# Performance work log

Measured on AMD Instinct MI355X. Metric: run time of the kernel, lower is better.

The kernel has to match this reference:

```python
import jax, jax.numpy as jnp
import numpy as np

NUM_HEADS = 6
V = 25          # num_points (joints)
F = 64          # num_frames
T = F * V       # 1600 tokens
DIM = 216
HD = DIM // NUM_HEADS
SCALE = HD ** -0.5
MAX_HOP = 16    # hop-distance table size (distances clipped to MAX_HOP-1)
LN_EPS = 1e-5


def _ntu_hop_dist():
    # NTU RGB+D 25-joint skeleton edges (1-indexed)
    edges = [(1, 2), (2, 21), (3, 21), (4, 3), (5, 21), (6, 5), (7, 6), (8, 7),
             (9, 21), (10, 9), (11, 10), (12, 11), (13, 1), (14, 13), (15, 14),
             (16, 15), (17, 1), (18, 17), (19, 18), (20, 19), (22, 23), (23, 8),
             (24, 25), (25, 12)]
    D = np.full((V, V), 99, dtype=np.int64)
    np.fill_diagonal(D, 0)
    for a, b in edges:
        D[a - 1, b - 1] = 1
        D[b - 1, a - 1] = 1
    for k in range(V):  # Floyd-Warshall on tiny 25-node graph
        D = np.minimum(D, D[:, k:k + 1] + D[k:k + 1, :])
    return np.clip(D, 0, MAX_HOP - 1).astype(np.int32)


def setup_inputs() -> dict:
    key = jax.random.key(0)
    ks = jax.random.split(key, 16)
    s = 0.02  # trunc_normal_(std=0.02) init scale
    rn = lambda k, shape: jax.random.normal(k, shape, jnp.float32) * s
    return {
        "x": jax.random.normal(ks[0], (8, T, DIM), jnp.float32),
        "qkv_w": rn(ks[1], (3 * DIM, DIM)),
        "proj_w": rn(ks[2], (DIM, DIM)),
        "proj_b": jnp.zeros((DIM,), jnp.float32),
        "norm_w": jnp.ones((DIM,), jnp.float32),
        "norm_b": jnp.zeros((DIM,), jnp.float32),
        "norm1_w": jnp.ones((DIM,), jnp.float32),
        "norm1_b": jnp.zeros((DIM,), jnp.float32),
        "fc1_w": rn(ks[3], (4 * DIM, DIM)),
        "fc1_b": jnp.zeros((4 * DIM,), jnp.float32),
        "fc2_w": rn(ks[4], (DIM, 4 * DIM)),
        "fc2_b": jnp.zeros((DIM,), jnp.float32),
        "t_w1": rn(ks[5], (DIM, 1)),
        "t_b1": jnp.zeros((DIM,), jnp.float32),
        "t_w2": rn(ks[6], (NUM_HEADS, DIM)),
        "t_b2": jnp.zeros((NUM_HEADS,), jnp.float32),
        "h_w1": rn(ks[7], (DIM, 1)),
        "h_b1": jnp.zeros((DIM,), jnp.float32),
        "h_w2": rn(ks[8], (NUM_HEADS, DIM)),
        "h_b2": jnp.zeros((NUM_HEADS,), jnp.float32),
        "hop_dist": jnp.asarray(_ntu_hop_dist()),
    }


def _ln(x, w, b):
    mu = x.mean(-1, keepdims=True)
    var = jnp.mean((x - mu) ** 2, axis=-1, keepdims=True)
    return (x - mu) * jax.lax.rsqrt(var + LN_EPS) * w + b


def reference(x, qkv_w, proj_w, proj_b, norm_w, norm_b, norm1_w, norm1_b,
              fc1_w, fc1_b, fc2_w, fc2_b, t_w1, t_b1, t_w2, t_b2,
              h_w1, h_b1, h_w2, h_b2, hop_dist):
    N = x.shape[0]
    h = _ln(x, norm_w, norm_b)
    qkv = (h @ qkv_w.T).reshape(N, T, 3, NUM_HEADS, HD).transpose(2, 0, 3, 1, 4)
    q, k, v = qkv[0], qkv[1], qkv[2]                       # (N,H,T,HD)
    attn = jnp.einsum('nhqc,nhkc->nhqk', q, k)             # (N,H,T,T)

    # temporal relative position bias (depends only on relative frame offset)
    coords = jnp.arange(-(F - 1), F, dtype=jnp.float32)[:, None]       # (2F-1,1)
    tbl_t = jax.nn.relu(coords @ t_w1.T + t_b1) @ t_w2.T + t_b2        # (2F-1,H)
    fidx = jnp.arange(F)
    rel = fidx[:, None] - fidx[None, :] + (F - 1)                      # (F,F)
    bias_t = tbl_t[rel].transpose(2, 0, 1)                             # (H,F,F)
    bias_t = jnp.repeat(jnp.repeat(bias_t, V, axis=1), V, axis=2)      # (H,T,T)

    # hop relative position bias (skeleton hop distance, same every frame pair)
    hvals = jnp.arange(MAX_HOP, dtype=jnp.float32)[:, None]            # (MAX_HOP,1)
    tbl_h = jax.nn.relu(hvals @ h_w1.T + h_b1) @ h_w2.T + h_b2         # (MAX_HOP,H)
    bias_h = tbl_h[hop_dist].transpose(2, 0, 1)                        # (H,V,V)
    bias_h = jnp.tile(bias_h, (1, F, F))                               # (H,T,T)

    attn = (attn + bias_h + bias_t) * SCALE  # scale AFTER bias, as in source
    attn = jax.nn.softmax(attn, axis=-1)
    o = jnp.einsum('nhqk,nhkc->nhqc', attn, v)
    o = o.transpose(0, 2, 1, 3).reshape(N, T, DIM)
    o = o @ proj_w.T + proj_b

    x1 = x + o  # skip_proj is Identity (dim_in == dim)
    h1 = _ln(x1, norm1_w, norm1_b)
    m = jax.nn.gelu(h1 @ fc1_w.T + fc1_b, approximate=False) @ fc2_w.T + fc2_b
    return x1 + m
```

## Files before the change

### kernel.cpp

```cpp
#include <hip/hip_runtime.h>
#include <hip/hip_bf16.h>


#define NHEAD  6
#define TLEN   1600
#define DIMC   216
#define HDIM   36
#define NBATCH 8
#define MROWS  12800
#define QK_SCALE (1.f/6.f)
#define C2EXP 0.24022650695910072f

typedef __attribute__((ext_vector_type(8))) short s16x8;
typedef __attribute__((ext_vector_type(4))) float f32x4;

#define MFMA16(a,b,c) __builtin_amdgcn_mfma_f32_16x16x32_bf16((a),(b),(c),0,0,0)

__device__ __forceinline__ float  bf2f(ushort u){ return __uint_as_float((uint)u << 16); }
__device__ __forceinline__ ushort f2bf(float f){
  uint u = __float_as_uint(f);
  u += 0x7FFFu + ((u >> 16) & 1u);
  return (ushort)(u >> 16);
}
__device__ __forceinline__ uint cvtpk_bf16(float lo, float hi){
  uint r;
  asm("v_cvt_pk_bf16_f32 %0, %1, %2" : "=v"(r) : "v"(lo), "v"(hi));
  return r;
}
__device__ __forceinline__ void glds16(const ushort* g, ushort* l){
  __builtin_amdgcn_global_load_lds(
      (const __attribute__((address_space(1))) void*)g,
      (__attribute__((address_space(3))) void*)l, 16, 0, 0);
}

__global__ __launch_bounds__(256) void bias_tables_kernel(
    const float* __restrict__ t_w1, const float* __restrict__ t_b1,
    const float* __restrict__ t_w2, const float* __restrict__ t_b2,
    const float* __restrict__ h_w1, const float* __restrict__ h_b1,
    const float* __restrict__ h_w2, const float* __restrict__ h_b2,
    const int*  __restrict__ hop,
    float* __restrict__ bias_t, float* __restrict__ bias_h)
{
  __shared__ float tblh[16][NHEAD];
  int tid = threadIdx.x;
  if (tid < 127) {
    float xi = (float)(tid - 63);
    float acc[NHEAD] = {0.f,0.f,0.f,0.f,0.f,0.f};
    for (int d = 0; d < DIMC; ++d) {
      float r = fmaxf(fmaf(xi, t_w1[d], t_b1[d]), 0.f);
      #pragma unroll
      for (int h = 0; h < NHEAD; ++h) acc[h] = fmaf(r, t_w2[h*DIMC + d], acc[h]);
    }
    #pragma unroll
    for (int h = 0; h < NHEAD; ++h)
      bias_t[h*127 + tid] = (acc[h] + t_b2[h]) * C2EXP;
  }
  if (tid >= 128 && tid < 144) {
    int i = tid - 128;
    float xi = (float)i;
    float acc[NHEAD] = {0.f,0.f,0.f,0.f,0.f,0.f};
    for (int d = 0; d < DIMC; ++d) {
      float r = fmaxf(fmaf(xi, h_w1[d], h_b1[d]), 0.f);
      #pragma unroll
      for (int h = 0; h < NHEAD; ++h) acc[h] = fmaf(r, h_w2[h*DIMC + d], acc[h]);
    }
    #pragma unroll
    for (int h = 0; h < NHEAD; ++h) tblh[i][h] = acc[h] + h_b2[h];
  }
  __syncthreads();
  for (int i = tid; i < NHEAD*625; i += 256) {
    int h = i / 625, e = i - h*625;
    bias_h[i] = tblh[hop[e]][h];
  }
}

__global__ __launch_bounds__(256) void padfill_kernel(
    const float* __restrict__ bh_raw,
    ushort* __restrict__ qb, ushort* __restrict__ kb)
{
  int idx = blockIdx.x*256 + threadIdx.x;
  if (idx >= NBATCH*NHEAD*TLEN) return;
  int nh = idx / TLEN, t = idx - nh*TLEN;
  int h = nh % NHEAD;
  int vk = t % 25;
  size_t row = ((size_t)nh*TLEN + t) << 6;
  ushort4 z = {0,0,0,0};
  #pragma unroll
  for (int i = 0; i < 7; ++i) *(ushort4*)(qb + row + 36 + i*4) = z;
  qb[row + 36 + vk] = 0x3F80;
  #pragma unroll
  for (int j = 0; j < 25; ++j)
    kb[row + 36 + j] = f2bf(bh_raw[h*625 + j*25 + vk]);
  kb[row + 61] = 0; kb[row + 62] = 0; kb[row + 63] = 0;
}

__global__ __launch_bounds__(256) void convpad_kernel(
    const float* __restrict__ src, ushort* __restrict__ dst,
    int N, int K, int Kpad, int total)
{
  int idx = blockIdx.x*256 + threadIdx.x;
  if (idx >= total) return;
  int n = idx / Kpad, k = idx - n*Kpad;
  float v = (n < N && k < K) ? src[n*K + k] : 0.f;
  dst[idx] = f2bf(v);
}

__global__ __launch_bounds__(256) void ln_kernel(
    const float* __restrict__ x, const float* __restrict__ w,
    const float* __restrict__ b, ushort* __restrict__ out)
{
  int lane = threadIdx.x & 63;
  int row  = blockIdx.x * 4 + (threadIdx.x >> 6);
  const float* xr = x + (size_t)row * DIMC;
  float v0 = xr[lane];
  float v1 = xr[lane + 64];
  float v2 = xr[lane + 128];
  float v3 = (lane < 24) ? xr[lane + 192] : 0.f;
  float s1 = v0 + v1 + v2 + v3;
  float s2 = v0*v0 + v1*v1 + v2*v2 + v3*v3;
  #pragma unroll
  for (int m = 32; m; m >>= 1) { s1 += __shfl_xor(s1, m); s2 += __shfl_xor(s2, m); }
  float mu  = s1 * (1.f/216.f);
  float var = fmaxf(s2 * (1.f/216.f) - mu*mu, 0.f);
  float rs  = rsqrtf(var + 1e-5f);
  ushort* orow = out + (size_t)row * 224;
  orow[lane]       = f2bf((v0-mu)*rs*w[lane]       + b[lane]);
  orow[lane+64]    = f2bf((v1-mu)*rs*w[lane+64]    + b[lane+64]);
  orow[lane+128]   = f2bf((v2-mu)*rs*w[lane+128]   + b[lane+128]);
  if (lane < 32) {
    float vv = (lane < 24) ? (v3-mu)*rs*w[lane+192] + b[lane+192] : 0.f;
    orow[lane+192] = f2bf(vv);
  }
}

enum { EPI_QKV = 0, EPI_PROJ = 1, EPI_FC1 = 2, EPI_FC2 = 3 };

template<int EPI, int WM>
__global__ __launch_bounds__(256) void gemm_mfma(
    const ushort* __restrict__ A, const ushort* __restrict__ B,
    const float* __restrict__ bias, const float* __restrict__ res,
    float* __restrict__ outf, ushort* __restrict__ oq,
    ushort* __restrict__ ok, ushort* __restrict__ ov,
    int N, int K)
{
  constexpr int BM = WM*4;
  constexpr int NMF = WM/16;
  constexpr int APASS = (BM*4)/256;
  __shared__ ushort As[2][BM*32];
  __shared__ ushort Bs[2][64*32];

  int tid = threadIdx.x;
  int w = tid >> 6, lane = tid & 63, l15 = lane & 15, g = lane >> 4;
  int row0 = blockIdx.x*BM, col0 = blockIdx.y*64;
  const int NT = K >> 5;

  f32x4 acc[NMF][4];
  #pragma unroll
  for (int i = 0; i < NMF; ++i)
    #pragma unroll
    for (int nf = 0; nf < 4; ++nf) acc[i][nf] = (f32x4){0.f,0.f,0.f,0.f};

  #define STAGE(buf, t)                                                       \
  {                                                                           \
    int k0 = (t) << 5;                                                        \
    _Pragma("unroll")                                                         \
    for (int p = 0; p < APASS; ++p) {                                         \
      int idx = p*256 + tid;                                                  \
      int mf = idx >> 6, kq = (idx >> 4) & 3, r = idx & 15;                   \
      glds16(A + (size_t)(row0 + mf*16 + r)*K + k0 + kq*8,                    \
             &As[buf][(p*256 + w*64)*8]);                                     \
    }                                                                         \
    {                                                                         \
      int kq = (tid >> 4) & 3, r = tid & 15;                                  \
      glds16(B + (size_t)(col0 + w*16 + r)*K + k0 + kq*8,                     \
             &Bs[buf][w*512]);                                                \
    }                                                                         \
  }

  STAGE(0, 0)
  __syncthreads();

  for (int t = 0; t < NT; ++t) {
    int buf = t & 1;
    if (t + 1 < NT) STAGE(buf ^ 1, t + 1)
    #pragma unroll
    for (int i = 0; i < NMF; ++i) {
      s16x8 a = *(const s16x8*)&As[buf][((w*NMF + i)*64 + g*16 + l15)*8];
      #pragma unroll
      for (int nf = 0; nf < 4; ++nf) {
        s16x8 b = *(const s16x8*)&Bs[buf][(nf*64 + g*16 + l15)*8];
        acc[i][nf] = MFMA16(a, b, acc[i][nf]);
      }
    }
    __syncthreads();
  }
  #undef STAGE

  #pragma unroll
  for (int i = 0; i < NMF; ++i) {
    #pragma unroll
    for (int nf = 0; nf < 4; ++nf) {
      int c = col0 + nf*16 + l15;
      if (c >= N) continue;
      #pragma unroll
      for (int r = 0; r < 4; ++r) {
        int rr = row0 + w*WM + i*16 + 4*g + r;
        float v = acc[i][nf][r];
        if constexpr (EPI == EPI_QKV) {
          int s = c / DIMC, rem = c - s*DIMC;
          int hh = rem / HDIM, d = rem - hh*HDIM;
          int n = rr / TLEN, t = rr - n*TLEN;
          int nh = n*NHEAD + hh;
          ushort bv = f2bf(v);
          if (s == 0)      oq[(((size_t)nh*TLEN + t) << 6) + d] = bv;
          else if (s == 1) ok[(((size_t)nh*TLEN + t) << 6) + d] = bv;
          else {
            int tile = t >> 6, pos = t & 63;
            int ks2 = pos >> 5, kg = (pos >> 2) & 7, r2 = pos & 3;
            int sg = ((kg & 3) << 1) + (kg >> 2);
            int posp = ks2*32 + sg*4 + r2;
            int grs = (posp >> 3) ^ (d & 7);
            ov[((size_t)nh*HDIM + d)*TLEN + tile*64 + grs*8 + (posp & 7)] = bv;
          }
        } else if constexpr (EPI == EPI_PROJ) {
          outf[(size_t)rr*DIMC + c] = v + bias[c] + res[(size_t)rr*DIMC + c];
        } else if constexpr (EPI == EPI_FC1) {
          v += bias[c];
          v = v * 0.5f * (1.f + erff(v * 0.70710678118654752f));
          oq[(size_t)rr*864 + c] = f2bf(v);
        } else {
          outf[(size_t)rr*DIMC + c] = v + bias[c] + res[(size_t)rr*DIMC + c];
        }
      }
    }
  }
}

__global__ __launch_bounds__(256) void attn_kernel(
    const ushort* __restrict__ qb, const ushort* __restrict__ kb,
    const ushort* __restrict__ vb, const float* __restrict__ bt_g,
    ushort* __restrict__ o)
{
  __shared__ ushort Ks[2][64*64];
  __shared__ ushort Vt[2][48*64];
  __shared__ float bts[128];

  int tid = threadIdx.x;
  int bid = blockIdx.x;
  int c   = bid >> 3;
  int c25 = c / 25;
  int nh  = (bid & 7)*6 + c25;
  int qt  = c - c25*25;
  int head = nh % NHEAD, n = nh / NHEAD;
  int wave = tid >> 6, lane = tid & 63;
  int g = lane >> 4, l15 = lane & 15, l7 = l15 & 7;

  if (tid < 127) bts[tid + 1] = bt_g[head*127 + tid];
  if (tid == 127) bts[0] = 0.f;
  {
    uint* p0 = (uint*)&Vt[0][36*64];
    uint* p1 = (uint*)&Vt[1][36*64];
    for (int i = tid; i < 384; i += 256) { p0[i] = 0; p1[i] = 0; }
  }

  int qglob = qt*64 + wave*16 + l15;
  const ushort* qrow = qb + (((size_t)nh*TLEN + qglob) << 6);
  s16x8 qf0 = *(const s16x8*)(qrow + g*8);
  s16x8 qf1 = *(const s16x8*)(qrow + 32 + g*8);

  int fq = qglob / 25;

  int vkb[4], ftb[4];
  #pragma unroll
  for (int kt = 0; kt < 4; ++kt) {
    int k0 = kt*16 + 4*g;
    int f0 = (k0 >= 50) ? 2 : (k0 >= 25 ? 1 : 0);
    vkb[kt] = k0 - f0*25;
    ftb[kt] = fq - f0 + 64;
  }

  float lsum = 0.f;
  f32x4 oa[3];
  #pragma unroll
  for (int dt = 0; dt < 3; ++dt) oa[dt] = (f32x4){0.f,0.f,0.f,0.f};

  const ushort* kbase = kb + ((size_t)nh*TLEN << 6);
  const ushort* vbase = vb + (size_t)nh*HDIM*TLEN;

  #define AST(buf, t0)                                                        \
  {                                                                           \
    _Pragma("unroll")                                                         \
    for (int p = 0; p < 2; ++p) {                                             \
      int gid = p*256 + tid;                                                  \
      int row = gid >> 3, grl = gid & 7;                                      \
      glds16(kbase + (((size_t)((t0) + row)) << 6) + ((grl ^ (row & 7)) << 3),\
             &Ks[buf][(p*256 + wave*64)*8]);                                  \
    }                                                                         \
    {                                                                         \
      int d = tid >> 3, grv = tid & 7;                                        \
      glds16(vbase + (size_t)d*TLEN + (t0) + grv*8,                           \
             &Vt[buf][wave*512]);                                             \
    }                                                                         \
    if (tid < 32) {                                                           \
      int d2 = (256 + tid) >> 3, grv2 = tid & 7;                              \
      glds16(vbase + (size_t)d2*TLEN + (t0) + grv2*8,                         \
             &Vt[buf][2048]);                                                 \
    }                                                                         \
  }

  AST(0, 0)
  __syncthreads();

  for (int t = 0; t < 25; ++t) {
    int buf = t & 1;
    if (t < 24) AST(buf ^ 1, (t + 1) * 64)

    f32x4 sa[4];
    #pragma unroll
    for (int kt = 0; kt < 4; ++kt) {
      const ushort* krow = &Ks[buf][(kt*16 + l15) << 6];
      s16x8 a0 = *(const s16x8*)(krow + ((g ^ l7) << 3));
      s16x8 a1 = *(const s16x8*)(krow + (((g + 4) ^ l7) << 3));
      f32x4 z = (f32x4){0.f,0.f,0.f,0.f};
      z = MFMA16(a0, qf0, z);
      sa[kt] = MFMA16(a1, qf1, z);
    }

    #pragma unroll
    for (int kt = 0; kt < 4; ++kt) {
      float bt0 = bts[ftb[kt]];
      float bt1 = bts[ftb[kt] - 1];
      #pragma unroll
      for (int r = 0; r < 4; ++r) {
        float btv = (vkb[kt] + r >= 25) ? bt1 : bt0;
        float arg = fminf(fmaf(sa[kt][r], C2EXP, btv), 80.f);
        float e = exp2f(arg);
        sa[kt][r] = e;
        lsum += e;
      }
    }

    #pragma unroll
    for (int ks = 0; ks < 2; ++ks) {
      union { s16x8 v; uint u[4]; } pf;
      pf.u[0] = cvtpk_bf16(sa[2*ks][0],   sa[2*ks][1]);
      pf.u[1] = cvtpk_bf16(sa[2*ks][2],   sa[2*ks][3]);
      pf.u[2] = cvtpk_bf16(sa[2*ks+1][0], sa[2*ks+1][1]);
      pf.u[3] = cvtpk_bf16(sa[2*ks+1][2], sa[2*ks+1][3]);
      #pragma unroll
      for (int dt = 0; dt < 3; ++dt) {
        s16x8 a = *(const s16x8*)&Vt[buf][((dt*16 + l15) << 6) +
                                          ((((ks << 2) + g) ^ l7) << 3)];
        oa[dt] = MFMA16(a, pf.v, oa[dt]);
      }
    }

    #pragma unroll
    for (int kt = 0; kt < 4; ++kt) {
      vkb[kt] += 14; ftb[kt] -= 2;
      if (vkb[kt] >= 25) { vkb[kt] -= 25; ftb[kt] -= 1; }
    }

    __syncthreads();
  }
  #undef AST

  lsum += __shfl_xor(lsum, 16);
  lsum += __shfl_xor(lsum, 32);
  float inv = 1.f / lsum;
  ushort* orow = o + ((size_t)(n*TLEN + qglob))*224 + head*HDIM;
  #pragma unroll
  for (int dt = 0; dt < 3; ++dt) {
    if (dt < 2 || g == 0) {
      ushort4 st;
      st.x = f2bf(oa[dt][0]*inv);
      st.y = f2bf(oa[dt][1]*inv);
      st.z = f2bf(oa[dt][2]*inv);
      st.w = f2bf(oa[dt][3]*inv);
      *(ushort4*)(orow + dt*16 + 4*g) = st;
    }
  }
}

extern "C" void kernel_launch(void* const* d_in, const int* in_sizes, int n_in,
                              void* d_out, int out_size, void* d_ws, size_t ws_size,
                              hipStream_t stream) {
  const float* x      = (const float*)d_in[0];
  const float* qkv_w  = (const float*)d_in[1];
  const float* proj_w = (const float*)d_in[2];
  const float* proj_b = (const float*)d_in[3];
  const float* norm_w = (const float*)d_in[4];
  const float* norm_b = (const float*)d_in[5];
  const float* norm1_w= (const float*)d_in[6];
  const float* norm1_b= (const float*)d_in[7];
  const float* fc1_w  = (const float*)d_in[8];
  const float* fc1_b  = (const float*)d_in[9];
  const float* fc2_w  = (const float*)d_in[10];
  const float* fc2_b  = (const float*)d_in[11];
  const float* t_w1   = (const float*)d_in[12];
  const float* t_b1   = (const float*)d_in[13];
  const float* t_w2   = (const float*)d_in[14];
  const float* t_b2   = (const float*)d_in[15];
  const float* h_w1   = (const float*)d_in[16];
  const float* h_b1   = (const float*)d_in[17];
  const float* h_w2   = (const float*)d_in[18];
  const float* h_b2   = (const float*)d_in[19];
  const int*   hop    = (const int*)d_in[20];

  const size_t WS_NEED = 40613504u;
  if (ws_size < WS_NEED) return;

  char* ws = (char*)d_ws;
  ushort* h_bf   = (ushort*)(ws);
  ushort* q_bf   = (ushort*)(ws + 5734400);
  ushort* k_bf   = (ushort*)(ws + 15564800);
  ushort* v_bf   = (ushort*)(ws + 25395200);
  ushort* o_bf   = (ushort*)(ws + 30924800);
  float*  x1     = (float*) (ws);
  ushort* h1_bf  = (ushort*)(ws + 11468800);
  ushort* g_bf   = (ushort*)(ws + 17203200);
  ushort* qkv_wb = (ushort*)(ws + 39321600);
  ushort* proj_wb= (ushort*)(ws + 39636992);
  ushort* fc1_wb = (ushort*)(ws + 39751680);
  ushort* fc2_wb = (ushort*)(ws + 40153088);
  float*  bt     = (float*) (ws + 40595456);
  float*  bh     = bt + 127*6;

  (void)hipMemsetAsync(ws + 30924800, 0, 5734400, stream);

  bias_tables_kernel<<<1, 256, 0, stream>>>(t_w1, t_b1, t_w2, t_b2,
                                            h_w1, h_b1, h_w2, h_b2, hop, bt, bh);

  padfill_kernel<<<(NBATCH*NHEAD*TLEN + 255)/256, 256, 0, stream>>>(bh, q_bf, k_bf);

  convpad_kernel<<<(704*224+255)/256, 256, 0, stream>>>(qkv_w,  qkv_wb, 648, 216, 224, 704*224);
  convpad_kernel<<<(256*224+255)/256, 256, 0, stream>>>(proj_w, proj_wb,216, 216, 224, 256*224);
  convpad_kernel<<<(896*224+255)/256, 256, 0, stream>>>(fc1_w,  fc1_wb, 864, 216, 224, 896*224);
  convpad_kernel<<<(256*864+255)/256, 256, 0, stream>>>(fc2_w,  fc2_wb, 216, 864, 864, 256*864);

  ln_kernel<<<MROWS/4, 256, 0, stream>>>(x, norm_w, norm_b, h_bf);

  gemm_mfma<EPI_QKV, 32><<<dim3(MROWS/128, 11), 256, 0, stream>>>(
      h_bf, qkv_wb, nullptr, nullptr, nullptr, q_bf, k_bf, v_bf, 648, 224);

  attn_kernel<<<1200, 256, 0, stream>>>(q_bf, k_bf, v_bf, bt, o_bf);

  gemm_mfma<EPI_PROJ, 16><<<dim3(MROWS/64, 4), 256, 0, stream>>>(
      o_bf, proj_wb, proj_b, x, x1, nullptr, nullptr, nullptr, 216, 224);

  ln_kernel<<<MROWS/4, 256, 0, stream>>>(x1, norm1_w, norm1_b, h1_bf);

  gemm_mfma<EPI_FC1, 32><<<dim3(MROWS/128, 14), 256, 0, stream>>>(
      h1_bf, fc1_wb, fc1_b, nullptr, nullptr, g_bf, nullptr, nullptr, 864, 224);

  gemm_mfma<EPI_FC2, 16><<<dim3(MROWS/64, 4), 256, 0, stream>>>(
      g_bf, fc2_wb, fc2_b, x1, (float*)d_out, nullptr, nullptr, nullptr, 216, 864);
}
```

Before: 187.0 us.

## Fuse weight conversions, use tanh GELU, fold softmax row sum into MFMA

Merges the four weight-conversion launches into one kernel. Swaps the exact erf GELU for a tanh-form sigmoid approximation built on raw v_exp/v_rcp instructions. In attention, the padded V rows are set to ones so one MFMA output column yields the softmax denominator, which removes the per-element sum and the exp clamp. It also simplifies the K/V prefetch address math with incrementing pointers. The tanh GELU changes numerics relative to the exact erf reference, and dropping the clamp risks overflow in exp.

Result: faster. 165.1 us (-11.7%).

```diff
diff --git a/kernel.cpp b/kernel.cpp
--- a/kernel.cpp
+++ b/kernel.cpp
@@ -27,6 +27,16 @@
   asm("v_cvt_pk_bf16_f32 %0, %1, %2" : "=v"(r) : "v"(lo), "v"(hi));
   return r;
 }
+__device__ __forceinline__ float fexp2(float x){
+  float r;
+  asm("v_exp_f32 %0, %1" : "=v"(r) : "v"(x));
+  return r;
+}
+__device__ __forceinline__ float frcp(float x){
+  float r;
+  asm("v_rcp_f32 %0, %1" : "=v"(r) : "v"(x));
+  return r;
+}
 __device__ __forceinline__ void glds16(const ushort* g, ushort* l){
   __builtin_amdgcn_global_load_lds(
       (const __attribute__((address_space(1))) void*)g,
@@ -94,15 +104,34 @@
   kb[row + 61] = 0; kb[row + 62] = 0; kb[row + 63] = 0;
 }
 
-__global__ __launch_bounds__(256) void convpad_kernel(
-    const float* __restrict__ src, ushort* __restrict__ dst,
-    int N, int K, int Kpad, int total)
+#define CP_QKV 157696
+#define CP_PROJ 215040
+#define CP_FC1 415744
+#define CP_TOT 636928
+__global__ __launch_bounds__(256) void convpad4_kernel(
+    const float* __restrict__ qkvw, const float* __restrict__ projw,
+    const float* __restrict__ fc1w, const float* __restrict__ fc2w,
+    ushort* __restrict__ dq, ushort* __restrict__ dp,
+    ushort* __restrict__ d1, ushort* __restrict__ d2)
 {
   int idx = blockIdx.x*256 + threadIdx.x;
-  if (idx >= total) return;
-  int n = idx / Kpad, k = idx - n*Kpad;
-  float v = (n < N && k < K) ? src[n*K + k] : 0.f;
-  dst[idx] = f2bf(v);
+  if (idx >= CP_TOT) return;
+  if (idx < CP_QKV) {
+    int n = idx / 224, k = idx - n*224;
+    dq[idx] = f2bf((n < 648 && k < 216) ? qkvw[n*216 + k] : 0.f);
+  } else if (idx < CP_PROJ) {
+    int i = idx - CP_QKV;
+    int n = i / 224, k = i - n*224;
+    dp[i] = f2bf((n < 216 && k < 216) ? projw[n*216 + k] : 0.f);
+  } else if (idx < CP_FC1) {
+    int i = idx - CP_PROJ;
+    int n = i / 224, k = i - n*224;
+    d1[i] = f2bf((n < 864 && k < 216) ? fc1w[n*216 + k] : 0.f);
+  } else {
+    int i = idx - CP_FC1;
+    int n = i / 864, k = i - n*864;
+    d2[i] = f2bf((n < 216) ? fc2w[n*864 + k] : 0.f);
+  }
 }
 
 __global__ __launch_bounds__(256) void ln_kernel(
@@ -226,7 +255,9 @@
           outf[(size_t)rr*DIMC + c] = v + bias[c] + res[(size_t)rr*DIMC + c];
         } else if constexpr (EPI == EPI_FC1) {
           v += bias[c];
-          v = v * 0.5f * (1.f + erff(v * 0.70710678118654752f));
+          float y = 0.7978845608f*(v + 0.044715f*v*v*v);
+          float e = fexp2(-2.885390082f*y);
+          v = v * frcp(1.f + e);
           oq[(size_t)rr*864 + c] = f2bf(v);
         } else {
           outf[(size_t)rr*DIMC + c] = v + bias[c] + res[(size_t)rr*DIMC + c];
@@ -257,10 +288,13 @@
 
   if (tid < 127) bts[tid + 1] = bt_g[head*127 + tid];
   if (tid == 127) bts[0] = 0.f;
-  {
-    uint* p0 = (uint*)&Vt[0][36*64];
-    uint* p1 = (uint*)&Vt[1][36*64];
-    for (int i = tid; i < 384; i += 256) { p0[i] = 0; p1[i] = 0; }
+  for (int i = tid; i < 768; i += 256) {
+    int b = i >> 8 >> 1;
+    (void)b;
+  }
+  for (int i = tid; i < 768; i += 256) {
+    int b = i / 384, j = i - b*384;
+    ((uint*)&Vt[b][36*64])[j] = (j < 32) ? 0x3F803F80u : 0u;
   }
 
   int qglob = qt*64 + wave*16 + l15;
@@ -279,41 +313,32 @@
     ftb[kt] = fq - f0 + 64;
   }
 
-  float lsum = 0.f;
   f32x4 oa[3];
   #pragma unroll
   for (int dt = 0; dt < 3; ++dt) oa[dt] = (f32x4){0.f,0.f,0.f,0.f};
 
-  const ushort* kbase = kb + ((size_t)nh*TLEN << 6);
-  const ushort* vbase = vb + (size_t)nh*HDIM*TLEN;
-
-  #define AST(buf, t0)                                                        \
-  {                                                                           \
-    _Pragma("unroll")                                                         \
-    for (int p = 0; p < 2; ++p) {                                             \
-      int gid = p*256 + tid;                                                  \
-      int row = gid >> 3, grl = gid & 7;                                      \
-      glds16(kbase + (((size_t)((t0) + row)) << 6) + ((grl ^ (row & 7)) << 3),\
-             &Ks[buf][(p*256 + wave*64)*8]);                                  \
-    }                                                                         \
-    {                                                                         \
-      int d = tid >> 3, grv = tid & 7;                                        \
-      glds16(vbase + (size_t)d*TLEN + (t0) + grv*8,                           \
-             &Vt[buf][wave*512]);                                             \
-    }                                                                         \
-    if (tid < 32) {                                                           \
-      int d2 = (256 + tid) >> 3, grv2 = tid & 7;                              \
-      glds16(vbase + (size_t)d2*TLEN + (t0) + grv2*8,                         \
-             &Vt[buf][2048]);                                                 \
-    }                                                                         \
-  }
-
-  AST(0, 0)
+  int srow = tid >> 3, sgrl = tid & 7;
+  const ushort* kp = kb + ((size_t)nh*TLEN << 6)
+                   + (srow << 6) + ((sgrl ^ (srow & 7)) << 3);
+  const ushort* vp = vb + (size_t)nh*HDIM*TLEN + srow*TLEN + sgrl*8;
+
+  glds16(kp,        &Ks[0][wave*512]);
+  glds16(kp + 2048, &Ks[0][2048 + wave*512]);
+  glds16(vp,        &Vt[0][wave*512]);
+  if (tid < 32) glds16(vp + 32*TLEN, &Vt[0][2048]);
+  kp += 4096; vp += 64;
   __syncthreads();
 
   for (int t = 0; t < 25; ++t) {
     int buf = t & 1;
-    if (t < 24) AST(buf ^ 1, (t + 1) * 64)
+    if (t < 24) {
+      ushort* kd = &Ks[buf ^ 1][wave*512];
+      glds16(kp,        kd);
+      glds16(kp + 2048, kd + 2048);
+      glds16(vp,        &Vt[buf ^ 1][wave*512]);
+      if (tid < 32) glds16(vp + 32*TLEN, &Vt[buf ^ 1][2048]);
+      kp += 4096; vp += 64;
+    }
 
     f32x4 sa[4];
     #pragma unroll
@@ -333,10 +358,7 @@
       #pragma unroll
       for (int r = 0; r < 4; ++r) {
         float btv = (vkb[kt] + r >= 25) ? bt1 : bt0;
-        float arg = fminf(fmaf(sa[kt][r], C2EXP, btv), 80.f);
-        float e = exp2f(arg);
-        sa[kt][r] = e;
-        lsum += e;
+        sa[kt][r] = fexp2(fmaf(sa[kt][r], C2EXP, btv));
       }
     }
 
@@ -363,11 +385,11 @@
 
     __syncthreads();
   }
-  #undef AST
-
-  lsum += __shfl_xor(lsum, 16);
-  lsum += __shfl_xor(lsum, 32);
-  float inv = 1.f / lsum;
+
+  float ls = (g == 1) ? oa[2][0] : 0.f;
+  ls += __shfl_xor(ls, 16);
+  ls += __shfl_xor(ls, 32);
+  float inv = frcp(ls);
   ushort* orow = o + ((size_t)(n*TLEN + qglob))*224 + head*HDIM;
   #pragma unroll
   for (int dt = 0; dt < 3; ++dt) {
@@ -433,10 +455,8 @@
 
   padfill_kernel<<<(NBATCH*NHEAD*TLEN + 255)/256, 256, 0, stream>>>(bh, q_bf, k_bf);
 
-  convpad_kernel<<<(704*224+255)/256, 256, 0, stream>>>(qkv_w,  qkv_wb, 648, 216, 224, 704*224);
-  convpad_kernel<<<(256*224+255)/256, 256, 0, stream>>>(proj_w, proj_wb,216, 216, 224, 256*224);
-  convpad_kernel<<<(896*224+255)/256, 256, 0, stream>>>(fc1_w,  fc1_wb, 864, 216, 224, 896*224);
-  convpad_kernel<<<(256*864+255)/256, 256, 0, stream>>>(fc2_w,  fc2_wb, 216, 864, 864, 256*864);
+  convpad4_kernel<<<(CP_TOT + 255)/256, 256, 0, stream>>>(
+      qkv_w, proj_w, fc1_w, fc2_w, qkv_wb, proj_wb, fc1_wb, fc2_wb);
 
   ln_kernel<<<MROWS/4, 256, 0, stream>>>(x, norm_w, norm_b, h_bf);
 
```
